# Kernel tuning notes

Measured on AMD Instinct MI355X. Metric: run time of the kernel, lower is better.

The kernel has to match this reference:

```python
import jax, jax.numpy as jnp
from jax import lax
import numpy as np

B, T, IN, H, OUT = 64, 512, 128, 512, 1


def _lstm_layer(x, W_ih, W_hh, b_ih, b_hh):
    # x: [B, T, in]; W_ih: [4H, in]; W_hh: [4H, H]; biases: [4H]
    # PyTorch gate order: i, f, g, o
    xg = jnp.einsum('bti,gi->btg', x, W_ih) + (b_ih + b_hh)  # [B, T, 4H]
    Hd = W_hh.shape[1]
    h0 = jnp.zeros((x.shape[0], Hd), x.dtype)

    def step(carry, xt):
        h, c = carry
        g = xt + h @ W_hh.T  # [B, 4H]
        i, f, gg, o = jnp.split(g, 4, axis=-1)
        i = jax.nn.sigmoid(i)
        f = jax.nn.sigmoid(f)
        gg = jnp.tanh(gg)
        o = jax.nn.sigmoid(o)
        c = f * c + i * gg
        h = o * jnp.tanh(c)
        return (h, c), h

    (_, _), hs = lax.scan(step, (h0, h0), jnp.swapaxes(xg, 0, 1))  # hs: [T, B, H]
    return jnp.swapaxes(hs, 0, 1)  # [B, T, H]


def setup_inputs() -> dict:
    key = jax.random.key(0)
    ks = jax.random.split(key, 11)
    s_in = 1.0 / np.sqrt(H)
    inp = {
        'x': jax.random.normal(ks[0], (B, T, IN), jnp.float32),
        'W_ih0': jax.random.uniform(ks[1], (4 * H, IN), jnp.float32, -s_in, s_in),
        'W_hh0': jax.random.uniform(ks[2], (4 * H, H), jnp.float32, -s_in, s_in),
        'b_ih0': jax.random.uniform(ks[3], (4 * H,), jnp.float32, -s_in, s_in),
        'b_hh0': jax.random.uniform(ks[4], (4 * H,), jnp.float32, -s_in, s_in),
        'W_ih1': jax.random.uniform(ks[5], (4 * H, H), jnp.float32, -s_in, s_in),
        'W_hh1': jax.random.uniform(ks[6], (4 * H, H), jnp.float32, -s_in, s_in),
        'b_ih1': jax.random.uniform(ks[7], (4 * H,), jnp.float32, -s_in, s_in),
        'b_hh1': jax.random.uniform(ks[8], (4 * H,), jnp.float32, -s_in, s_in),
        'Wl': jax.random.uniform(ks[9], (OUT, H), jnp.float32, -s_in, s_in),
        'bl': jax.random.uniform(ks[10], (OUT,), jnp.float32, -s_in, s_in),
    }
    return inp


def reference(x, W_ih0, W_hh0, b_ih0, b_hh0, W_ih1, W_hh1, b_ih1, b_hh1, Wl, bl):
    h = _lstm_layer(x, W_ih0, W_hh0, b_ih0, b_hh0)   # layer 0
    h = _lstm_layer(h, W_ih1, W_hh1, b_ih1, b_hh1)   # layer 1
    last = h[:, -1, :]                                # [B, H]
    out = last @ Wl.T + bl                            # [B, OUT]; classification=False -> no sigmoid
    return out
```

## Files before the change

### kernel.cpp

```cpp
#include <hip/hip_runtime.h>
#include <cmath>

#define TT 512
#define BB 64
#define HH 512
#define II 128
#define NBLK 256

typedef float v2f __attribute__((ext_vector_type(2)));
__device__ __forceinline__ v2f fma2(v2f a, v2f b, v2f c) { return __builtin_elementwise_fma(a, b, c); }

#define SMEM_FLOATS (16384 + 16384 + 1024 + 256 + 16)
#define SMEM_BYTES  (SMEM_FLOATS * 4)

__device__ __forceinline__ float fexp2(float x) { float r; asm("v_exp_f32 %0, %1" : "=v"(r) : "v"(x)); return r; }
__device__ __forceinline__ float frcpf(float x) { float r; asm("v_rcp_f32 %0, %1" : "=v"(r) : "v"(x)); return r; }
__device__ __forceinline__ float sigm(float v)  { return frcpf(1.0f + fexp2(-1.44269504f * v)); }
__device__ __forceinline__ float ftanh(float v) { return __builtin_fmaf(2.0f, frcpf(1.0f + fexp2(-2.88539008f * v)), -1.0f); }

__device__ __forceinline__ unsigned umin2(unsigned a, unsigned b) { return a < b ? a : b; }
#define CBAR() asm volatile("" ::: "memory")

template<int KN>
__device__ __forceinline__ void loadh2b(const float* __restrict__ src, int k0,
                                        int bp, v2f (&v)[KN]) {
#pragma unroll
  for (int i = 0; i < KN; ++i)
    v[i] = *(const v2f*)(src + (size_t)(k0 + i) * BB + 2 * bp);
}
template<int KN>
__device__ __forceinline__ void loadx2(const float* __restrict__ src, int k0,
                                       int bp, v2f (&v)[KN]) {
#pragma unroll
  for (int i = 0; i < KN; ++i)
    v[i] = *(const v2f*)(src + (size_t)(k0 + i) * BB + 2 * bp);
}

__device__ __forceinline__ void step2(const float* wk8, v2f h2, v2f (&acc)[8]) {
  const float4* wp = (const float4*)wk8;
  const float4 w0 = wp[0], w1 = wp[1];
  acc[0] = fma2((v2f){w0.x, w0.x}, h2, acc[0]);
  acc[1] = fma2((v2f){w0.y, w0.y}, h2, acc[1]);
  acc[2] = fma2((v2f){w0.z, w0.z}, h2, acc[2]);
  acc[3] = fma2((v2f){w0.w, w0.w}, h2, acc[3]);
  acc[4] = fma2((v2f){w1.x, w1.x}, h2, acc[4]);
  acc[5] = fma2((v2f){w1.y, w1.y}, h2, acc[5]);
  acc[6] = fma2((v2f){w1.z, w1.z}, h2, acc[6]);
  acc[7] = fma2((v2f){w1.w, w1.w}, h2, acc[7]);
}
template<int KN>
__device__ __forceinline__ void consume2(const float* __restrict__ wro, int k0,
                                         const v2f (&v)[KN], v2f (&acc)[8]) {
#pragma unroll
  for (int i = 0; i < KN; ++i) step2(wro + (size_t)(k0 + i) * 16, v[i], acc);
}

__device__ __forceinline__ void span32(const float* __restrict__ src,
                                       const float* __restrict__ wro,
                                       int k0, int bp, v2f (&acc)[8]) {
  v2f a[4], b[4];
  loadh2b<4>(src, k0,      bp, a);
  loadh2b<4>(src, k0 + 4,  bp, b);
  consume2<4>(wro, k0,      a, acc);
  loadh2b<4>(src, k0 + 8,  bp, a);
  consume2<4>(wro, k0 + 4,  b, acc);
  loadh2b<4>(src, k0 + 12, bp, b);
  consume2<4>(wro, k0 + 8,  a, acc);
  loadh2b<4>(src, k0 + 16, bp, a);
  consume2<4>(wro, k0 + 12, b, acc);
  loadh2b<4>(src, k0 + 20, bp, b);
  consume2<4>(wro, k0 + 16, a, acc);
  loadh2b<4>(src, k0 + 24, bp, a);
  consume2<4>(wro, k0 + 20, b, acc);
  loadh2b<4>(src, k0 + 28, bp, b);
  consume2<4>(wro, k0 + 24, a, acc);
  consume2<4>(wro, k0 + 28, b, acc);
}

__global__ __launch_bounds__(1024) void k_transpose_x(const float* __restrict__ x,
                                                      float* __restrict__ xT) {
  __shared__ float tile[64][65];
  const int t  = blockIdx.x >> 1;
  const int k0 = (blockIdx.x & 1) << 6;
  const int lk = threadIdx.x & 63;
  const int lb = threadIdx.x >> 6;
#pragma unroll
  for (int bp = 0; bp < 64; bp += 16) {
    const int b = bp + lb;
    tile[lk][b] = x[((size_t)b * TT + t) * II + k0 + lk];
  }
  __syncthreads();
  const int b2  = threadIdx.x & 63;
  const int kk0 = threadIdx.x >> 6;
#pragma unroll
  for (int kp = 0; kp < 64; kp += 16) {
    const int kk = kp + kk0;
    xT[((size_t)t * II + k0 + kk) * BB + b2] = tile[kk][b2];
  }
}

__global__ void k_init_flags(unsigned* flags) { flags[threadIdx.x] = 0u; }

__global__ __launch_bounds__(1024, 4) void k_lstm_persist(
    const float* __restrict__ xT,
    const float* __restrict__ W_ih0, const float* __restrict__ W_hh0,
    const float* __restrict__ b_ih0, const float* __restrict__ b_hh0,
    const float* __restrict__ W_ih1, const float* __restrict__ W_hh1,
    const float* __restrict__ b_ih1, const float* __restrict__ b_hh1,
    float* __restrict__ h0ring, float* __restrict__ h1ring,
    unsigned* __restrict__ flags)
{
  extern __shared__ float smem[];
  float* wlds  = smem;
  float* part  = wlds + 16384;
  float* gates = part + 16384;
  float* cst   = gates + 1024;
  float* bsum  = cst + 256;

  const int bid = blockIdx.x;
  const int L   = bid >> 7;
  const int ub  = (bid & 127) << 2;
  const int tid = threadIdx.x;

  const float* WA = L ? W_ih1 : W_ih0;
  const float* WB = L ? W_hh1 : W_hh0;
  const int KA = L ? HH : II;

  const int ktot = KA + HH;
  for (int idx = tid; idx < 16 * ktot; idx += 1024) {
    const int k  = idx >> 4;
    const int lr = idx & 15;
    const int u = lr >> 2, q = lr & 3;
    const int G = q * HH + ub + u;
    wlds[idx] = (k < KA) ? WA[G * KA + k] : WB[G * HH + (k - KA)];
  }
  if (tid < 16) {
    const int u = tid >> 2, q = tid & 3;
    const int G = q * HH + ub + u;
    bsum[tid] = L ? (b_ih1[G] + b_hh1[G]) : (b_ih0[G] + b_hh0[G]);
  }
  if (tid < 256) cst[tid] = 0.0f;
  __syncthreads();

  const int bp    = tid & 31;
  const int rhalf = (tid >> 5) & 1;
  const int kseg  = tid >> 6;

  const float* wroA  = wlds + rhalf * 8;
  const float* wroB0 = wlds + (size_t)II * 16 + rhalf * 8;
  const float* wroB1 = wlds + (size_t)HH * 16 + rhalf * 8;

  for (int s = 0; s <= TT; ++s) {
    const int t = L ? (s - 1) : s;
    const bool active = (t >= 0 && t < TT);
    const bool first  = (t == 0);

    v2f acc[8];
#pragma unroll
    for (int j = 0; j < 8; ++j) acc[j] = (v2f){0.0f, 0.0f};

    if (active && L == 0) {
      v2f xa[4], xb[4];
      const float* xp = xT + (size_t)t * (II * BB);
      loadx2<4>(xp, kseg * 8,     bp, xa);
      loadx2<4>(xp, kseg * 8 + 4, bp, xb);
      consume2<4>(wroA, kseg * 8,     xa, acc);
      consume2<4>(wroA, kseg * 8 + 4, xb, acc);
    }

    if (s > 0) {
      if (tid < 64) {
        const unsigned tgt = (unsigned)s;
        for (;;) {
          const unsigned m0 = __hip_atomic_load(flags + tid,       __ATOMIC_RELAXED, __HIP_MEMORY_SCOPE_AGENT);
          const unsigned m1 = __hip_atomic_load(flags + tid +  64, __ATOMIC_RELAXED, __HIP_MEMORY_SCOPE_AGENT);
          const unsigned m2 = __hip_atomic_load(flags + tid + 128, __ATOMIC_RELAXED, __HIP_MEMORY_SCOPE_AGENT);
          const unsigned m3 = __hip_atomic_load(flags + tid + 192, __ATOMIC_RELAXED, __HIP_MEMORY_SCOPE_AGENT);
          const unsigned mn = umin2(umin2(m0, m1), umin2(m2, m3));
          if (__all(mn >= tgt)) break;
          __builtin_amdgcn_s_sleep(1);
        }
        __builtin_amdgcn_fence(__ATOMIC_ACQUIRE, "agent");
      }
      __syncthreads();
      CBAR();
    }

    if (active) {
      if (L == 0) {
        if (!first) {
          span32(h0ring + (size_t)((s - 1) & 1) * (HH * BB),
                 wroB0, kseg * 32, bp, acc);
        }
      } else {
        span32(h0ring + (size_t)((s - 1) & 1) * (HH * BB),
               wroA, kseg * 32, bp, acc);
        if (!first) {
          span32(h1ring + (size_t)(s & 1) * (HH * BB),
                 wroB1, kseg * 32, bp, acc);
        }
      }

#pragma unroll
      for (int j = 0; j < 8; ++j) {
        const int row = rhalf * 8 + j;
        *(v2f*)(part + ((((size_t)row * 16 + kseg) * 32 + bp) << 1)) = acc[j];
      }
      __syncthreads();
      {
        const int row = tid >> 6;
        const int bb  = tid & 63;
        float g = 0.0f;
#pragma unroll
        for (int ks = 0; ks < 16; ++ks)
          g += part[((((size_t)row * 16 + ks) * 32 + (bb >> 1)) << 1) + (bb & 1)];
        gates[row * 64 + bb] = g + bsum[row];
      }
      __syncthreads();

      if (tid < 256) {
        const int u = tid >> 6, bb = tid & 63;
        const float gi = sigm(gates[((u << 2) + 0) * 64 + bb]);
        const float gf = sigm(gates[((u << 2) + 1) * 64 + bb]);
        const float gg = ftanh(gates[((u << 2) + 2) * 64 + bb]);
        const float go = sigm(gates[((u << 2) + 3) * 64 + bb]);
        const float cold = first ? 0.0f : cst[u * 64 + bb];
        const float cn = gf * cold + gi * gg;
        const float hn = go * ftanh(cn);
        cst[u * 64 + bb] = cn;
        float* hdst = (L ? h1ring : h0ring) + (size_t)(t & 1) * (HH * BB);
        float old = __hip_atomic_exchange(hdst + (ub + u) * 64 + bb, hn,
                                          __ATOMIC_RELAXED, __HIP_MEMORY_SCOPE_AGENT);
        asm volatile("" :: "v"(old));
      }
    }

    __syncthreads();
    if (tid == 0 && s < TT) {
      __hip_atomic_store(flags + bid, (unsigned)(s + 1),
                         __ATOMIC_RELAXED, __HIP_MEMORY_SCOPE_AGENT);
    }
  }
}

__global__ __launch_bounds__(512) void k_final(const float* __restrict__ h1last,
                                               const float* __restrict__ Wl,
                                               const float* __restrict__ bl,
                                               float* __restrict__ out) {
  __shared__ float red[8][64];
  const int jg = threadIdx.x >> 6, b = threadIdx.x & 63;
  float a = 0.0f;
  for (int jj = 0; jj < 64; ++jj) {
    const int j = (jg << 6) + jj;
    a += h1last[j * BB + b] * Wl[j];
  }
  red[jg][b] = a;
  __syncthreads();
  if (threadIdx.x < 64) {
    float s = bl[0];
#pragma unroll
    for (int g = 0; g < 8; ++g) s += red[g][threadIdx.x];
    out[threadIdx.x] = s;
  }
}

extern "C" void kernel_launch(void* const* d_in, const int* in_sizes, int n_in,
                              void* d_out, int out_size, void* d_ws, size_t ws_size,
                              hipStream_t stream) {
  (void)in_sizes; (void)n_in; (void)out_size; (void)ws_size;
  const float* x     = (const float*)d_in[0];
  const float* W_ih0 = (const float*)d_in[1];
  const float* W_hh0 = (const float*)d_in[2];
  const float* b_ih0 = (const float*)d_in[3];
  const float* b_hh0 = (const float*)d_in[4];
  const float* W_ih1 = (const float*)d_in[5];
  const float* W_hh1 = (const float*)d_in[6];
  const float* b_ih1 = (const float*)d_in[7];
  const float* b_hh1 = (const float*)d_in[8];
  const float* Wl    = (const float*)d_in[9];
  const float* bl    = (const float*)d_in[10];
  float* out = (float*)d_out;

  float* ws       = (float*)d_ws;
  float* xT       = ws;
  float* h0ring   = xT + (size_t)TT * II * BB;
  float* h1ring   = h0ring + 2 * HH * BB;
  unsigned* flags = (unsigned*)(h1ring + 2 * HH * BB);

  k_transpose_x<<<1024, 1024, 0, stream>>>(x, xT);
  k_init_flags<<<1, NBLK, 0, stream>>>(flags);

  hipFuncSetAttribute((const void*)k_lstm_persist,
                      hipFuncAttributeMaxDynamicSharedMemorySize, SMEM_BYTES);

  void* args[] = {
    (void*)&xT,
    (void*)&W_ih0, (void*)&W_hh0, (void*)&b_ih0, (void*)&b_hh0,
    (void*)&W_ih1, (void*)&W_hh1, (void*)&b_ih1, (void*)&b_hh1,
    (void*)&h0ring, (void*)&h1ring, (void*)&flags,
  };
  hipLaunchCooperativeKernel((void*)k_lstm_persist, dim3(NBLK), dim3(1024),
                             args, SMEM_BYTES, stream);

  k_final<<<1, 512, 0, stream>>>(h1ring + HH * BB, Wl, bl, out);
}
```

Before: 7.890 ms.

## Stream recurrent hidden state into LDS via async global_load_lds pipeline

Replaces per-thread register loads of the h-ring vectors in the recurrent matvec with direct global-to-LDS loads into a 4-slot per-wave staging buffer, using manual vmcnt waits to keep up to four 4-row chunks in flight. Each wave loads a chunk once and its two row-half lanes share it, instead of each lane fetching its own pairs from global memory. The partial-sum layout is changed so the staging area reuses the part buffer, and the reduction indexing is updated to match. This adds hand-written waitcnt and sched barriers, plus a full vmcnt drain before the step barrier, which may serialize more than before.

```diff
diff --git a/kernel.cpp b/kernel.cpp
--- a/kernel.cpp
+++ b/kernel.cpp
@@ -21,19 +21,22 @@
 __device__ __forceinline__ unsigned umin2(unsigned a, unsigned b) { return a < b ? a : b; }
 #define CBAR() asm volatile("" ::: "memory")
 
-template<int KN>
-__device__ __forceinline__ void loadh2b(const float* __restrict__ src, int k0,
-                                        int bp, v2f (&v)[KN]) {
-#pragma unroll
-  for (int i = 0; i < KN; ++i)
-    v[i] = *(const v2f*)(src + (size_t)(k0 + i) * BB + 2 * bp);
-}
-template<int KN>
-__device__ __forceinline__ void loadx2(const float* __restrict__ src, int k0,
-                                       int bp, v2f (&v)[KN]) {
-#pragma unroll
-  for (int i = 0; i < KN; ++i)
-    v[i] = *(const v2f*)(src + (size_t)(k0 + i) * BB + 2 * bp);
+__device__ __forceinline__ void waitvm(int n) {
+  if (n == 0)      { asm volatile("s_waitcnt vmcnt(0)" ::: "memory"); }
+  else if (n == 1) { asm volatile("s_waitcnt vmcnt(1)" ::: "memory"); }
+  else if (n == 2) { asm volatile("s_waitcnt vmcnt(2)" ::: "memory"); }
+  else             { asm volatile("s_waitcnt vmcnt(3)" ::: "memory"); }
+  __builtin_amdgcn_sched_barrier(0);
+}
+__device__ __forceinline__ void lds_reads_done() {
+  asm volatile("s_waitcnt lgkmcnt(0)" ::: "memory");
+  __builtin_amdgcn_sched_barrier(0);
+}
+
+__device__ __forceinline__ void gll16(const float* g, float* lds_dst) {
+  __builtin_amdgcn_global_load_lds(
+      (const __attribute__((address_space(1))) void*)g,
+      (__attribute__((address_space(3))) void*)lds_dst, 16, 0, 0);
 }
 
 __device__ __forceinline__ void step2(const float* wk8, v2f h2, v2f (&acc)[8]) {
@@ -48,6 +51,14 @@
   acc[6] = fma2((v2f){w1.z, w1.z}, h2, acc[6]);
   acc[7] = fma2((v2f){w1.w, w1.w}, h2, acc[7]);
 }
+
+template<int KN>
+__device__ __forceinline__ void loadx2(const float* __restrict__ src, int k0,
+                                       int bp, v2f (&v)[KN]) {
+#pragma unroll
+  for (int i = 0; i < KN; ++i)
+    v[i] = *(const v2f*)(src + (size_t)(k0 + i) * BB + 2 * bp);
+}
 template<int KN>
 __device__ __forceinline__ void consume2(const float* __restrict__ wro, int k0,
                                          const v2f (&v)[KN], v2f (&acc)[8]) {
@@ -55,26 +66,39 @@
   for (int i = 0; i < KN; ++i) step2(wro + (size_t)(k0 + i) * 16, v[i], acc);
 }
 
-__device__ __forceinline__ void span32(const float* __restrict__ src,
-                                       const float* __restrict__ wro,
-                                       int k0, int bp, v2f (&acc)[8]) {
-  v2f a[4], b[4];
-  loadh2b<4>(src, k0,      bp, a);
-  loadh2b<4>(src, k0 + 4,  bp, b);
-  consume2<4>(wro, k0,      a, acc);
-  loadh2b<4>(src, k0 + 8,  bp, a);
-  consume2<4>(wro, k0 + 4,  b, acc);
-  loadh2b<4>(src, k0 + 12, bp, b);
-  consume2<4>(wro, k0 + 8,  a, acc);
-  loadh2b<4>(src, k0 + 16, bp, a);
-  consume2<4>(wro, k0 + 12, b, acc);
-  loadh2b<4>(src, k0 + 20, bp, b);
-  consume2<4>(wro, k0 + 16, a, acc);
-  loadh2b<4>(src, k0 + 24, bp, a);
-  consume2<4>(wro, k0 + 20, b, acc);
-  loadh2b<4>(src, k0 + 28, bp, b);
-  consume2<4>(wro, k0 + 24, a, acc);
-  consume2<4>(wro, k0 + 28, b, acc);
+template<int NB0, int NB1>
+__device__ __forceinline__ void spans_gll(
+    const float* __restrict__ srcA, const float* __restrict__ wroA_,
+    const float* __restrict__ srcB, const float* __restrict__ wroB_,
+    float* __restrict__ stage, int kbase, int lane, int bp, v2f (&acc)[8]) {
+  constexpr int NB = NB0 + NB1;
+#pragma unroll
+  for (int i = 0; i < 4 && i < NB; ++i) {
+    const float* src = (i < NB0) ? srcA : srcB;
+    const int ii = (i < NB0) ? i : i - NB0;
+    gll16(src + (size_t)(kbase + 4 * ii) * BB + lane * 4, stage + (i & 3) * 256);
+  }
+#pragma unroll
+  for (int i = 0; i < NB; ++i) {
+    const int rem = NB - 1 - i;
+    waitvm(rem < 3 ? rem : 3);
+    const float* wro = (i < NB0) ? wroA_ : wroB_;
+    const int ii = (i < NB0) ? i : i - NB0;
+    const int k = kbase + 4 * ii;
+    const float* slot = stage + (i & 3) * 256;
+#pragma unroll
+    for (int kl = 0; kl < 4; ++kl) {
+      v2f h2 = *(const v2f*)(slot + kl * 64 + bp * 2);
+      step2(wro + (size_t)(k + kl) * 16, h2, acc);
+    }
+    if (i + 4 < NB) {
+      lds_reads_done();
+      const int j = i + 4;
+      const float* src = (j < NB0) ? srcA : srcB;
+      const int jj = (j < NB0) ? j : j - NB0;
+      gll16(src + (size_t)(kbase + 4 * jj) * BB + lane * 4, stage + (j & 3) * 256);
+    }
+  }
 }
 
 __global__ __launch_bounds__(1024) void k_transpose_x(const float* __restrict__ x,
@@ -142,6 +166,7 @@
   if (tid < 256) cst[tid] = 0.0f;
   __syncthreads();
 
+  const int lane  = tid & 63;
   const int bp    = tid & 31;
   const int rhalf = (tid >> 5) & 1;
   const int kseg  = tid >> 6;
@@ -149,6 +174,7 @@
   const float* wroA  = wlds + rhalf * 8;
   const float* wroB0 = wlds + (size_t)II * 16 + rhalf * 8;
   const float* wroB1 = wlds + (size_t)HH * 16 + rhalf * 8;
+  float* stage = part + (size_t)kseg * 1024;
 
   for (int s = 0; s <= TT; ++s) {
     const int t = L ? (s - 1) : s;
@@ -187,24 +213,25 @@
     }
 
     if (active) {
+      const float* h0src = h0ring + (size_t)((s - 1) & 1) * (HH * BB);
       if (L == 0) {
-        if (!first) {
-          span32(h0ring + (size_t)((s - 1) & 1) * (HH * BB),
-                 wroB0, kseg * 32, bp, acc);
-        }
+        if (!first)
+          spans_gll<8, 0>(h0src, wroB0, nullptr, nullptr,
+                          stage, kseg * 32, lane, bp, acc);
       } else {
-        span32(h0ring + (size_t)((s - 1) & 1) * (HH * BB),
-               wroA, kseg * 32, bp, acc);
-        if (!first) {
-          span32(h1ring + (size_t)(s & 1) * (HH * BB),
-                 wroB1, kseg * 32, bp, acc);
-        }
+        const float* h1src = h1ring + (size_t)(s & 1) * (HH * BB);
+        if (first)
+          spans_gll<8, 0>(h0src, wroA, nullptr, nullptr,
+                          stage, kseg * 32, lane, bp, acc);
+        else
+          spans_gll<8, 8>(h0src, wroA, h1src, wroB1,
+                          stage, kseg * 32, lane, bp, acc);
       }
 
 #pragma unroll
       for (int j = 0; j < 8; ++j) {
         const int row = rhalf * 8 + j;
-        *(v2f*)(part + ((((size_t)row * 16 + kseg) * 32 + bp) << 1)) = acc[j];
+        *(v2f*)(part + (size_t)kseg * 1024 + row * 64 + bp * 2) = acc[j];
       }
       __syncthreads();
       {
@@ -213,7 +240,7 @@
         float g = 0.0f;
 #pragma unroll
         for (int ks = 0; ks < 16; ++ks)
-          g += part[((((size_t)row * 16 + ks) * 32 + (bb >> 1)) << 1) + (bb & 1)];
+          g += part[(size_t)ks * 1024 + row * 64 + bb];
         gates[row * 64 + bb] = g + bsum[row];
       }
       __syncthreads();
@@ -235,6 +262,7 @@
       }
     }
 
+    asm volatile("s_waitcnt vmcnt(0)" ::: "memory");
     __syncthreads();
     if (tid == 0 && s < TT) {
       __hip_atomic_store(flags + bid, (unsigned)(s + 1),
```

Measured after the change: 7.445 ms. -5.6%, faster.
